# Optimization experiments

Hardware: AMD Instinct MI355X
Metric: run time of the kernel (lower is better)

The kernel has to match this reference:

```python
import jax, jax.numpy as jnp
import numpy as np

EMBED_DIM = 384
HEADS = 6
HEAD_DIM = EMBED_DIM // HEADS
WINDOW = 64


def setup_inputs() -> dict:
    key = jax.random.key(0)
    ks = jax.random.split(key, 5)
    B, T = 128, 256
    s_attn = 1.0 / np.sqrt(EMBED_DIM)
    x = jax.random.normal(ks[0], (B, T, EMBED_DIM), dtype=jnp.float32)
    W_attn = jax.random.normal(ks[1], (EMBED_DIM, 3 * EMBED_DIM), dtype=jnp.float32) * s_attn
    b_attn = jax.random.normal(ks[2], (3 * EMBED_DIM,), dtype=jnp.float32) * 0.02
    W_proj = jax.random.normal(ks[3], (EMBED_DIM, EMBED_DIM), dtype=jnp.float32) * s_attn
    b_proj = jax.random.normal(ks[4], (EMBED_DIM,), dtype=jnp.float32) * 0.02
    return {"x": x, "W_attn": W_attn, "b_attn": b_attn, "W_proj": W_proj, "b_proj": b_proj}


def reference(x, W_attn, b_attn, W_proj, b_proj):
    B, T, C = x.shape
    qkv = x @ W_attn + b_attn  # [B,T,3C]
    q, k, v = jnp.split(qkv, 3, axis=-1)
    # [B, H, T, hd]
    q = q.reshape(B, T, HEADS, HEAD_DIM).transpose(0, 2, 1, 3)
    k = k.reshape(B, T, HEADS, HEAD_DIM).transpose(0, 2, 1, 3)
    v = v.reshape(B, T, HEADS, HEAD_DIM).transpose(0, 2, 1, 3)
    scale = 1.0 / np.sqrt(HEAD_DIM).astype(np.float32)
    att = jnp.einsum('bhqd,bhkd->bhqk', q, k) * scale
    i = jnp.arange(T)
    causal = i[:, None] >= i[None, :]
    local = jnp.abs(i[:, None] - i[None, :]) <= WINDOW
    mask = (causal & local)[None, None, :, :]
    att = jnp.where(mask, att, -jnp.inf)
    att = jax.nn.softmax(att, axis=-1)
    y = jnp.einsum('bhqk,bhkd->bhqd', att, v)
    y = y.transpose(0, 2, 1, 3).reshape(B, T, C)
    return y @ W_proj + b_proj
```

## Files before the change

kernel.cpp:

```cpp
#include <hip/hip_runtime.h>

#define B_SZ   128
#define T_SEQ  256
#define C_DIM  384
#define HEADS  6
#define HD     64
#define WIN    64

typedef __bf16 bf16x8 __attribute__((ext_vector_type(8)));
typedef float  f32x4  __attribute__((ext_vector_type(4)));

typedef __attribute__((address_space(3))) void lds_void;
typedef __attribute__((address_space(1))) void gbl_void;

__device__ __forceinline__ unsigned short f2bf(float f) {
  unsigned u = __float_as_uint(f);
  u += 0x7FFFu + ((u >> 16) & 1u);
  return (unsigned short)(u >> 16);
}

__global__ __launch_bounds__(256) void convert_f32_bf16(
    const float* __restrict__ in, unsigned short* __restrict__ out, int n4) {
  int i = blockIdx.x * blockDim.x + threadIdx.x;
  if (i < n4) {
    float4 v = ((const float4*)in)[i];
    ushort4 o;
    o.x = f2bf(v.x); o.y = f2bf(v.y); o.z = f2bf(v.z); o.w = f2bf(v.w);
    ((ushort4*)out)[i] = o;
  }
}

__global__ __launch_bounds__(256) void transpose_convert(
    const float* __restrict__ in, unsigned short* __restrict__ out,
    int K, int N) {
  __shared__ float tile[32][33];
  const int gx = blockIdx.x * 32;
  const int gy = blockIdx.y * 32;
  const int tx = threadIdx.x;
  const int ty = threadIdx.y;
#pragma unroll
  for (int r = ty; r < 32; r += 8)
    tile[r][tx] = in[(size_t)(gy + r) * N + gx + tx];
  __syncthreads();
#pragma unroll
  for (int r = ty; r < 32; r += 8)
    out[(size_t)(gx + r) * K + gy + tx] = f2bf(tile[tx][r]);
}

template <bool OUT_BF16, int KK>
__global__ __launch_bounds__(256, 3) void gemm_mfma_bf16(
    const unsigned short* __restrict__ A,
    const unsigned short* __restrict__ Bt,
    const float* __restrict__ bias,
    void* __restrict__ Cv, int M, int N, int tiles_n) {
  __shared__ __attribute__((aligned(16))) char smem_raw[49152];
  float* ep = (float*)smem_raw;

  constexpr int NK = KK / 32;

  const int t    = threadIdx.x;
  const int lane = t & 63;
  const int w    = t >> 6;
  const int wr   = w >> 1;
  const int wc   = w & 1;

  const unsigned id    = blockIdx.x;
  const unsigned remap = (id & 7u) * (gridDim.x >> 3) + (id >> 3);
  const int by = remap / (unsigned)tiles_n;
  const int bx = remap % (unsigned)tiles_n;
  const int m0 = by * 128;
  const int n0 = bx * 128;

  const int lrow = lane >> 2;
  const int lcol = lane & 3;
  const int sc   = lcol ^ ((lrow >> 1) & 3);

  const int m16  = lane & 15;
  const int quad = lane >> 4;
  const int cp   = (quad ^ ((m16 >> 1) & 3)) << 3;

  f32x4 acc[4][4];
#pragma unroll
  for (int i = 0; i < 4; ++i)
#pragma unroll
    for (int j = 0; j < 4; ++j) acc[i][j] = (f32x4){0.f, 0.f, 0.f, 0.f};

  auto stage = [&](int slot, int k0) {
    unsigned short* Ad = (unsigned short*)(smem_raw + slot * 16384);
    unsigned short* Bd = Ad + 128 * 32;
#pragma unroll
    for (int i = 0; i < 2; ++i) {
      const int inst = w * 2 + i;
      const int r = inst * 16 + lrow;
      const unsigned short* ga = A + (size_t)(m0 + r) * KK + k0 + sc * 8;
      __builtin_amdgcn_global_load_lds((const gbl_void*)ga,
                                       (lds_void*)(Ad + inst * 512), 16, 0, 0);
    }
#pragma unroll
    for (int i = 0; i < 2; ++i) {
      const int inst = w * 2 + i;
      const int r = inst * 16 + lrow;
      const unsigned short* gb = Bt + (size_t)(n0 + r) * KK + k0 + sc * 8;
      __builtin_amdgcn_global_load_lds((const gbl_void*)gb,
                                       (lds_void*)(Bd + inst * 512), 16, 0, 0);
    }
  };

  stage(0, 0);
  stage(1, 32);

#pragma unroll
  for (int kt = 0; kt < NK; ++kt) {
    if (kt + 1 < NK)
      asm volatile("s_waitcnt vmcnt(4)" ::: "memory");
    else
      asm volatile("s_waitcnt vmcnt(0)" ::: "memory");
    __builtin_amdgcn_s_barrier();
    __builtin_amdgcn_sched_barrier(0);

    if (kt + 2 < NK) stage((kt + 2) % 3, (kt + 2) * 32);

    const unsigned short* Ac =
        (const unsigned short*)(smem_raw + (kt % 3) * 16384);
    const unsigned short* Bc = Ac + 128 * 32;

    bf16x8 af[4];
#pragma unroll
    for (int mt = 0; mt < 4; ++mt)
      af[mt] = *(const bf16x8*)(Ac + (size_t)(wr * 64 + mt * 16 + m16) * 32 + cp);
#pragma unroll
    for (int nt = 0; nt < 4; ++nt) {
      bf16x8 bfr = *(const bf16x8*)(Bc + (size_t)(wc * 64 + nt * 16 + m16) * 32 + cp);
#pragma unroll
      for (int mt = 0; mt < 4; ++mt)
        acc[mt][nt] = __builtin_amdgcn_mfma_f32_16x16x32_bf16(
            af[mt], bfr, acc[mt][nt], 0, 0, 0);
    }
  }
  __syncthreads();

  float bv[4];
#pragma unroll
  for (int nt = 0; nt < 4; ++nt) bv[nt] = bias[n0 + wc * 64 + nt * 16 + m16];

#pragma unroll
  for (int p = 0; p < 2; ++p) {
    if (p) __syncthreads();
    if (wr == p) {
#pragma unroll
      for (int mt = 0; mt < 4; ++mt)
#pragma unroll
        for (int nt = 0; nt < 4; ++nt)
#pragma unroll
          for (int r = 0; r < 4; ++r)
            ep[(mt * 16 + quad * 4 + r) * 132 + wc * 64 + nt * 16 + m16] =
                acc[mt][nt][r] + bv[nt];
    }
    __syncthreads();
#pragma unroll
    for (int cc = 0; cc < 8; ++cc) {
      const int chunk = cc * 256 + t;
      const int row = chunk >> 5;
      const int c4  = chunk & 31;
      f32x4 v = *(const f32x4*)(ep + row * 132 + c4 * 4);
      const int grow = m0 + p * 64 + row;
      const int gcol = n0 + c4 * 4;
      if (OUT_BF16) {
        ushort4 o;
        o.x = f2bf(v[0]); o.y = f2bf(v[1]); o.z = f2bf(v[2]); o.w = f2bf(v[3]);
        *(ushort4*)((unsigned short*)Cv + (size_t)grow * N + gcol) = o;
      } else {
        *(f32x4*)((float*)Cv + (size_t)grow * N + gcol) = v;
      }
    }
  }
}

#define PSTR 68
__global__ __launch_bounds__(256) void attn_mfma(
    const unsigned short* __restrict__ qkv, unsigned short* __restrict__ y) {
  __shared__ unsigned short Qs[64 * 64];
  __shared__ unsigned short Ks[64 * 64];
  __shared__ unsigned short Vt[64 * 64];
  __shared__ float Pw[4][16 * PSTR];

  const unsigned id  = blockIdx.x;
  const unsigned bid = (id & 7u) * (gridDim.x >> 3) + (id >> 3);
  const int qt  = bid & 3;
  const int h   = (bid >> 2) % HEADS;
  const int b   = bid / (4 * HEADS);
  const int t   = threadIdx.x;
  const int lane = t & 63;
  const int w    = t >> 6;
  const int quad = lane >> 4;
  const int m16  = lane & 15;
  const int sw   = m16 & 7;

  const size_t rowbase = (size_t)b * T_SEQ * (3 * C_DIM);
  const int qoff = h * HD;
  const int koff = C_DIM + h * HD;
  const int voff = 2 * C_DIM + h * HD;
  const int qg0  = qt * 64;

  const int lrow = lane >> 3;
  const int lcol = lane & 7;
  const int schunk = lcol ^ lrow;

#pragma unroll
  for (int i = 0; i < 2; ++i) {
    const int inst = w * 2 + i;
    const int r = inst * 8 + lrow;
    const unsigned short* ga =
        qkv + rowbase + (size_t)(qg0 + r) * (3 * C_DIM) + qoff + schunk * 8;
    __builtin_amdgcn_global_load_lds((const gbl_void*)ga,
                                     (lds_void*)(Qs + inst * 512), 16, 0, 0);
  }

  float m_r[4], l_r[4];
  f32x4 yacc[4];
#pragma unroll
  for (int r = 0; r < 4; ++r) { m_r[r] = -1e30f; l_r[r] = 0.f; }
#pragma unroll
  for (int dt = 0; dt < 4; ++dt) yacc[dt] = (f32x4){0.f, 0.f, 0.f, 0.f};

  const int nchunks  = (qt == 0) ? 1 : 2;
  const int kb_first = (qt == 0) ? 0 : (qg0 - 64);
  const int qrow_base = qg0 + w * 16 + quad * 4;

  for (int ch = 0; ch < nchunks; ++ch) {
    const int kb = kb_first + ch * 64;

    __syncthreads();

#pragma unroll
    for (int i = 0; i < 2; ++i) {
      const int inst = w * 2 + i;
      const int r = inst * 8 + lrow;
      const unsigned short* ga =
          qkv + rowbase + (size_t)(kb + r) * (3 * C_DIM) + koff + schunk * 8;
      __builtin_amdgcn_global_load_lds((const gbl_void*)ga,
                                       (lds_void*)(Ks + inst * 512), 16, 0, 0);
    }
    {
      const int vkey = t & 63;
      const int kc = vkey >> 3, ke = vkey & 7;
      const int vd0  = (t >> 6) * 16;
      const unsigned short* gv =
          qkv + rowbase + (size_t)(kb + vkey) * (3 * C_DIM) + voff + vd0;
#pragma unroll
      for (int u = 0; u < 4; ++u) {
        ushort4 vv = *(const ushort4*)(gv + u * 4);
#pragma unroll
        for (int jj = 0; jj < 4; ++jj) {
          const int d = vd0 + u * 4 + jj;
          const unsigned short val =
              (jj == 0) ? vv.x : (jj == 1) ? vv.y : (jj == 2) ? vv.z : vv.w;
          Vt[d * 64 + ((kc ^ (d & 7)) << 3) + ke] = val;
        }
      }
    }
    __syncthreads();

    f32x4 sacc[4];
#pragma unroll
    for (int nt = 0; nt < 4; ++nt) sacc[nt] = (f32x4){0.f, 0.f, 0.f, 0.f};
#pragma unroll
    for (int ks = 0; ks < 64; ks += 32) {
      const int cp = (((ks >> 3) + quad) ^ sw) << 3;
      bf16x8 aq = *(const bf16x8*)(Qs + (size_t)(w * 16 + m16) * 64 + cp);
#pragma unroll
      for (int nt = 0; nt < 4; ++nt) {
        bf16x8 kf = *(const bf16x8*)(Ks + (size_t)(nt * 16 + m16) * 64 + cp);
        sacc[nt] = __builtin_amdgcn_mfma_f32_16x16x32_bf16(aq, kf, sacc[nt], 0, 0, 0);
      }
    }

    float mc[4] = {-1e30f, -1e30f, -1e30f, -1e30f};
#pragma unroll
    for (int nt = 0; nt < 4; ++nt) {
      const int kg = kb + nt * 16 + m16;
#pragma unroll
      for (int r = 0; r < 4; ++r) {
        const int qg = qrow_base + r;
        const bool valid = (kg <= qg) && (qg - kg <= WIN);
        const float sv = valid ? (sacc[nt][r] * 0.125f) : -1e30f;
        sacc[nt][r] = sv;
        mc[r] = fmaxf(mc[r], sv);
      }
    }
#pragma unroll
    for (int r = 0; r < 4; ++r) {
#pragma unroll
      for (int x = 1; x <= 8; x <<= 1) mc[r] = fmaxf(mc[r], __shfl_xor(mc[r], x));
    }

#pragma unroll
    for (int r = 0; r < 4; ++r) {
      const float mn    = fmaxf(m_r[r], mc[r]);
      const float alpha = __expf(m_r[r] - mn);
      m_r[r] = mn;
      l_r[r] *= alpha;
#pragma unroll
      for (int dt = 0; dt < 4; ++dt) yacc[dt][r] *= alpha;
      float ls = 0.f;
#pragma unroll
      for (int nt = 0; nt < 4; ++nt) {
        const float p = __expf(sacc[nt][r] - mn);
        sacc[nt][r] = p;
        ls += p;
      }
#pragma unroll
      for (int x = 1; x <= 8; x <<= 1) ls += __shfl_xor(ls, x);
      l_r[r] += ls;
    }

#pragma unroll
    for (int nt = 0; nt < 4; ++nt)
#pragma unroll
      for (int r = 0; r < 4; ++r)
        Pw[w][(quad * 4 + r) * PSTR + nt * 16 + m16] = sacc[nt][r];

#pragma unroll
    for (int ks = 0; ks < 64; ks += 32) {
      f32x4 pa = *(const f32x4*)(&Pw[w][m16 * PSTR + ks + quad * 8]);
      f32x4 pb = *(const f32x4*)(&Pw[w][m16 * PSTR + ks + quad * 8 + 4]);
      bf16x8 ap;
#pragma unroll
      for (int j = 0; j < 4; ++j) {
        ap[j]     = (__bf16)pa[j];
        ap[4 + j] = (__bf16)pb[j];
      }
      const int cp = (((ks >> 3) + quad) ^ sw) << 3;
#pragma unroll
      for (int dt = 0; dt < 4; ++dt) {
        bf16x8 vf = *(const bf16x8*)(Vt + (size_t)(dt * 16 + m16) * 64 + cp);
        yacc[dt] = __builtin_amdgcn_mfma_f32_16x16x32_bf16(ap, vf, yacc[dt], 0, 0, 0);
      }
    }
  }

  float* epy = &Pw[0][0];
  float inv[4];
#pragma unroll
  for (int r = 0; r < 4; ++r) inv[r] = 1.f / l_r[r];
#pragma unroll
  for (int dt = 0; dt < 4; ++dt)
#pragma unroll
    for (int r = 0; r < 4; ++r)
      epy[(w * 16 + quad * 4 + r) * PSTR + dt * 16 + m16] = yacc[dt][r] * inv[r];
  __syncthreads();
#pragma unroll
  for (int cc = 0; cc < 4; ++cc) {
    const int chunk = cc * 256 + t;
    const int row = chunk >> 4;
    const int c4  = chunk & 15;
    f32x4 v = *(const f32x4*)(epy + row * PSTR + c4 * 4);
    ushort4 o;
    o.x = f2bf(v[0]); o.y = f2bf(v[1]); o.z = f2bf(v[2]); o.w = f2bf(v[3]);
    *(ushort4*)(y + (size_t)(b * T_SEQ + qg0 + row) * C_DIM + h * HD + c4 * 4) = o;
  }
}

extern "C" void kernel_launch(void* const* d_in, const int* in_sizes, int n_in,
                              void* d_out, int out_size, void* d_ws, size_t ws_size,
                              hipStream_t stream) {
  const float* x      = (const float*)d_in[0];
  const float* W_attn = (const float*)d_in[1];
  const float* b_attn = (const float*)d_in[2];
  const float* W_proj = (const float*)d_in[3];
  const float* b_proj = (const float*)d_in[4];
  float* out = (float*)d_out;

  const int M = B_SZ * T_SEQ;

  unsigned short* qkv_b = (unsigned short*)d_ws;
  unsigned short* y_b   = qkv_b + (size_t)M * (3 * C_DIM);
  unsigned short* x_b   = y_b   + (size_t)M * C_DIM;
  unsigned short* Wa_t  = x_b   + (size_t)M * C_DIM;
  unsigned short* Wp_t  = Wa_t  + (size_t)(3 * C_DIM) * C_DIM;

  {
    int n4 = M * C_DIM / 4;
    convert_f32_bf16<<<n4 / 256, 256, 0, stream>>>(x, x_b, n4);
    transpose_convert<<<dim3((3 * C_DIM) / 32, C_DIM / 32), dim3(32, 8), 0, stream>>>(
        W_attn, Wa_t, C_DIM, 3 * C_DIM);
    transpose_convert<<<dim3(C_DIM / 32, C_DIM / 32), dim3(32, 8), 0, stream>>>(
        W_proj, Wp_t, C_DIM, C_DIM);
  }

  gemm_mfma_bf16<true, C_DIM><<<dim3(9 * (M / 128)), 256, 0, stream>>>(
      x_b, Wa_t, b_attn, qkv_b, M, 3 * C_DIM, 9);

  attn_mfma<<<dim3(B_SZ * HEADS * (T_SEQ / 64)), 256, 0, stream>>>(qkv_b, y_b);

  gemm_mfma_bf16<false, C_DIM><<<dim3(3 * (M / 128)), 256, 0, stream>>>(
      y_b, Wp_t, b_proj, out, M, C_DIM, 3);
}
```

Baseline: 201.7 us.

## Pre-pack GEMM operands into swizzled contiguous tile layout for LDS loads

The bf16 conversion kernels and the attention epilogue now write the GEMM operands (x, weights, attention output y) in a blocked layout: 128-row by 32-column tiles stored contiguously with the LDS XOR swizzle already applied. The GEMM staging then issues fully contiguous global_load_lds reads per wave instead of strided row gathers, which should improve memory coalescing and simplify address arithmetic. The conversion kernels gain more complex index math and scattered ushort4 stores, and the attention kernel's output stores become less contiguous. The qkv layout used by attention is unchanged.

```diff
diff --git a/kernel.cpp b/kernel.cpp
--- a/kernel.cpp
+++ b/kernel.cpp
@@ -19,18 +19,27 @@
   return (unsigned short)(u >> 16);
 }
 
-__global__ __launch_bounds__(256) void convert_f32_bf16(
-    const float* __restrict__ in, unsigned short* __restrict__ out, int n4) {
-  int i = blockIdx.x * blockDim.x + threadIdx.x;
-  if (i < n4) {
-    float4 v = ((const float4*)in)[i];
-    ushort4 o;
-    o.x = f2bf(v.x); o.y = f2bf(v.y); o.z = f2bf(v.z); o.w = f2bf(v.w);
-    ((ushort4*)out)[i] = o;
-  }
-}
-
-__global__ __launch_bounds__(256) void transpose_convert(
+
+__global__ __launch_bounds__(256) void convert_pack_f32_bf16(
+    const float* __restrict__ in, unsigned short* __restrict__ out) {
+  const int tid = blockIdx.x * 256 + threadIdx.x;
+  const int m   = tid / 48;
+  const int rem = tid % 48;
+  const int kc  = rem >> 2;
+  const int u   = rem & 3;
+  const float4 a = *(const float4*)(in + (size_t)m * 384 + kc * 32 + u * 8);
+  const float4 b = *(const float4*)(in + (size_t)m * 384 + kc * 32 + u * 8 + 4);
+  const int p = u ^ ((m & 7) >> 1);
+  unsigned short* dst =
+      out + ((size_t)(m >> 7) * 12 + kc) * 4096 + (m & 127) * 32 + p * 8;
+  ushort4 o1, o2;
+  o1.x = f2bf(a.x); o1.y = f2bf(a.y); o1.z = f2bf(a.z); o1.w = f2bf(a.w);
+  o2.x = f2bf(b.x); o2.y = f2bf(b.y); o2.z = f2bf(b.z); o2.w = f2bf(b.w);
+  *(ushort4*)dst = o1;
+  *(ushort4*)(dst + 4) = o2;
+}
+
+__global__ __launch_bounds__(256) void transpose_convert_pack(
     const float* __restrict__ in, unsigned short* __restrict__ out,
     int K, int N) {
   __shared__ float tile[32][33];
@@ -42,9 +51,15 @@
   for (int r = ty; r < 32; r += 8)
     tile[r][tx] = in[(size_t)(gy + r) * N + gx + tx];
   __syncthreads();
-#pragma unroll
-  for (int r = ty; r < 32; r += 8)
-    out[(size_t)(gx + r) * K + gy + tx] = f2bf(tile[tx][r]);
+  const int nkc = K >> 5;
+#pragma unroll
+  for (int r = ty; r < 32; r += 8) {
+    const int n = gx + r;
+    const int k = gy + tx;
+    const int p = (((k >> 3) & 3) ^ ((n & 7) >> 1));
+    out[((size_t)(n >> 7) * nkc + (k >> 5)) * 4096 + (n & 127) * 32 + p * 8 +
+        (k & 7)] = f2bf(tile[tx][r]);
+  }
 }
 
 template <bool OUT_BF16, int KK>
@@ -71,9 +86,8 @@
   const int m0 = by * 128;
   const int n0 = bx * 128;
 
-  const int lrow = lane >> 2;
-  const int lcol = lane & 3;
-  const int sc   = lcol ^ ((lrow >> 1) & 3);
+  const unsigned short* Atile = A  + (size_t)by * NK * 4096;
+  const unsigned short* Btile = Bt + (size_t)bx * NK * 4096;
 
   const int m16  = lane & 15;
   const int quad = lane >> 4;
@@ -85,40 +99,36 @@
 #pragma unroll
     for (int j = 0; j < 4; ++j) acc[i][j] = (f32x4){0.f, 0.f, 0.f, 0.f};
 
-  auto stage = [&](int slot, int k0) {
+  auto stage = [&](int slot, int kc) {
     unsigned short* Ad = (unsigned short*)(smem_raw + slot * 16384);
     unsigned short* Bd = Ad + 128 * 32;
+    const unsigned short* ta = Atile + (size_t)kc * 4096;
+    const unsigned short* tb = Btile + (size_t)kc * 4096;
 #pragma unroll
     for (int i = 0; i < 2; ++i) {
       const int inst = w * 2 + i;
-      const int r = inst * 16 + lrow;
-      const unsigned short* ga = A + (size_t)(m0 + r) * KK + k0 + sc * 8;
-      __builtin_amdgcn_global_load_lds((const gbl_void*)ga,
-                                       (lds_void*)(Ad + inst * 512), 16, 0, 0);
-    }
-#pragma unroll
-    for (int i = 0; i < 2; ++i) {
-      const int inst = w * 2 + i;
-      const int r = inst * 16 + lrow;
-      const unsigned short* gb = Bt + (size_t)(n0 + r) * KK + k0 + sc * 8;
-      __builtin_amdgcn_global_load_lds((const gbl_void*)gb,
-                                       (lds_void*)(Bd + inst * 512), 16, 0, 0);
+      __builtin_amdgcn_global_load_lds(
+          (const gbl_void*)(ta + inst * 512 + lane * 8),
+          (lds_void*)(Ad + inst * 512), 16, 0, 0);
+      __builtin_amdgcn_global_load_lds(
+          (const gbl_void*)(tb + inst * 512 + lane * 8),
+          (lds_void*)(Bd + inst * 512), 16, 0, 0);
     }
   };
 
   stage(0, 0);
-  stage(1, 32);
+  stage(1, 1);
 
 #pragma unroll
   for (int kt = 0; kt < NK; ++kt) {
     if (kt + 1 < NK)
-      asm volatile("s_waitcnt vmcnt(4)" ::: "memory");
+      asm volatile("s_waitcnt vmcnt(4) lgkmcnt(0)" ::: "memory");
     else
-      asm volatile("s_waitcnt vmcnt(0)" ::: "memory");
+      asm volatile("s_waitcnt vmcnt(0) lgkmcnt(0)" ::: "memory");
     __builtin_amdgcn_s_barrier();
     __builtin_amdgcn_sched_barrier(0);
 
-    if (kt + 2 < NK) stage((kt + 2) % 3, (kt + 2) * 32);
+    if (kt + 2 < NK) stage((kt + 2) % 3, kt + 2);
 
     const unsigned short* Ac =
         (const unsigned short*)(smem_raw + (kt % 3) * 16384);
@@ -357,7 +367,13 @@
     f32x4 v = *(const f32x4*)(epy + row * PSTR + c4 * 4);
     ushort4 o;
     o.x = f2bf(v[0]); o.y = f2bf(v[1]); o.z = f2bf(v[2]); o.w = f2bf(v[3]);
-    *(ushort4*)(y + (size_t)(b * T_SEQ + qg0 + row) * C_DIM + h * HD + c4 * 4) = o;
+    const int m = b * T_SEQ + qg0 + row;
+    const int c = h * HD + c4 * 4;
+    const int kc = c >> 5;
+    const int u  = (c >> 3) & 3;
+    const int p  = u ^ ((m & 7) >> 1);
+    *(ushort4*)(y + ((size_t)(m >> 7) * 12 + kc) * 4096 + (m & 127) * 32 +
+                p * 8 + (c & 7)) = o;
   }
 }
 
@@ -380,12 +396,11 @@
   unsigned short* Wp_t  = Wa_t  + (size_t)(3 * C_DIM) * C_DIM;
 
   {
-    int n4 = M * C_DIM / 4;
-    convert_f32_bf16<<<n4 / 256, 256, 0, stream>>>(x, x_b, n4);
-    transpose_convert<<<dim3((3 * C_DIM) / 32, C_DIM / 32), dim3(32, 8), 0, stream>>>(
-        W_attn, Wa_t, C_DIM, 3 * C_DIM);
-    transpose_convert<<<dim3(C_DIM / 32, C_DIM / 32), dim3(32, 8), 0, stream>>>(
-        W_proj, Wp_t, C_DIM, C_DIM);
+    convert_pack_f32_bf16<<<dim3(M * 48 / 256), 256, 0, stream>>>(x, x_b);
+    transpose_convert_pack<<<dim3((3 * C_DIM) / 32, C_DIM / 32), dim3(32, 8), 0,
+                             stream>>>(W_attn, Wa_t, C_DIM, 3 * C_DIM);
+    transpose_convert_pack<<<dim3(C_DIM / 32, C_DIM / 32), dim3(32, 8), 0,
+                             stream>>>(W_proj, Wp_t, C_DIM, C_DIM);
   }
 
   gemm_mfma_bf16<true, C_DIM><<<dim3(9 * (M / 128)), 256, 0, stream>>>(
```

Result: faster. 191.5 us (-5.1%).
